# Kernel optimization log

Measured on AMD Instinct MI355X. Metric: run time of the kernel, lower is better.

The kernel has to match this reference:

```python
import jax, jax.numpy as jnp
import numpy as np

EPS = 1e-9

def squash(s, axis=-1):
    # v = (|s|^2 / (1+|s|^2)) * s/|s|
    sq_norm = jnp.sum(s * s, axis=axis, keepdims=True)
    scale = sq_norm / (1.0 + sq_norm) / jnp.sqrt(sq_norm + EPS)
    return scale * s

def setup_inputs() -> dict:
    key = jax.random.key(0)
    k1, k2 = jax.random.split(key)
    B, N, Din = 256, 1152, 8   # batch, input caps, input cap dim
    C, U = 10, 16              # output caps, output cap dim
    inputs = jax.random.normal(k1, (B, N, Din), dtype=jnp.float32)
    # 'uniform' keras initializer ~ U(-0.05, 0.05)
    W = jax.random.uniform(k2, (C, N, Din, U), dtype=jnp.float32, minval=-0.05, maxval=0.05)
    return {"inputs": inputs, "W": W}

ROUTING_ITERATIONS = 3

def reference(inputs, W):
    B = inputs.shape[0]
    C = W.shape[0]
    N = W.shape[1]
    # prediction vectors u_hat: (B, C, N, U)
    u_hat = jnp.einsum('bni,cniu->bcnu', inputs, W)
    # coupling logits b: ones, shape (B, C, N) (trailing singleton dropped)
    b = jnp.ones((B, C, N), dtype=inputs.dtype)
    out = None
    for i in range(ROUTING_ITERATIONS):
        # softmax over input-capsule axis (axis=-2 of (B,C,N,1) == N)
        c = jax.nn.softmax(b, axis=-1)  # (B, C, N)
        s = jnp.einsum('bcnu,bcn->bcu', u_hat, c)  # weighted sum over input caps
        out = squash(s, axis=-1)  # (B, C, U)
        if i < ROUTING_ITERATIONS - 1:
            # agreement: u_hat . v
            b = b + jnp.einsum('bcnu,bcu->bcn', u_hat, out)
    return out
```

## Files before the change

kernel.cpp:

```cpp
#include <hip/hip_runtime.h>
#include <math.h>


#define BATCH 256
#define CAPS  10
#define NIN   1152
#define DIN   8
#define UDIM  16
#define TPB   512
#define KITER 9

__global__ __launch_bounds__(TPB, 1) void capsule_routing_kernel(
    const float* __restrict__ x,
    const float* __restrict__ W,
    float* __restrict__ out)
{
    const int gblk = blockIdx.x;
    const int c    = gblk >> 8;
    const int b    = gblk & 255;
    const int t    = threadIdx.x;
    const int ub   = (t & 3) << 2;
    const int gg   = t >> 2;
    const int wave = t >> 6;

    __shared__ float x_s[NIN * DIN];
    __shared__ float b_s[NIN];
    __shared__ float redB[8];
    __shared__ float ps[8][UDIM];
    __shared__ float v_s[UDIM];

    {
        const float4* xg = (const float4*)(x + (size_t)b * (NIN * DIN));
        float4* xs = (float4*)x_s;
        #pragma unroll
        for (int i = 0; i < 5; ++i) {
            const int idx = t + TPB * i;
            if (idx < (NIN * DIN / 4)) xs[idx] = xg[idx];
        }
    }
    for (int n = t; n < NIN; n += TPB) b_s[n] = 1.0f;
    __syncthreads();

    const float* Wc = W + (size_t)c * (NIN * DIN * UDIM);

    float4 uh0, uh1, uh2, uh3, uh4, uh5, uh6, uh7, uh8;

#define UHCOMP(K, DST) { \
    const int n = gg + 128 * (K); \
    const float4* wr = (const float4*)(Wc + n * (DIN * UDIM) + ub); \
    const float4 xa = ((const float4*)(x_s + n * DIN))[0]; \
    const float4 xb = ((const float4*)(x_s + n * DIN))[1]; \
    float4 w0 = wr[0], w1 = wr[4], w2 = wr[8], w3 = wr[12]; \
    float4 acc; \
    acc.x = xa.x * w0.x + xa.y * w1.x + xa.z * w2.x + xa.w * w3.x; \
    acc.y = xa.x * w0.y + xa.y * w1.y + xa.z * w2.y + xa.w * w3.y; \
    acc.z = xa.x * w0.z + xa.y * w1.z + xa.z * w2.z + xa.w * w3.z; \
    acc.w = xa.x * w0.w + xa.y * w1.w + xa.z * w2.w + xa.w * w3.w; \
    w0 = wr[16]; w1 = wr[20]; w2 = wr[24]; w3 = wr[28]; \
    acc.x += xb.x * w0.x + xb.y * w1.x + xb.z * w2.x + xb.w * w3.x; \
    acc.y += xb.x * w0.y + xb.y * w1.y + xb.z * w2.y + xb.w * w3.y; \
    acc.z += xb.x * w0.z + xb.y * w1.z + xb.z * w2.z + xb.w * w3.z; \
    acc.w += xb.x * w0.w + xb.y * w1.w + xb.z * w2.w + xb.w * w3.w; \
    DST = acc; } \
    __builtin_amdgcn_sched_barrier(0);

    UHCOMP(0, uh0)
    UHCOMP(1, uh1)
    UHCOMP(2, uh2)
    UHCOMP(3, uh3)
    UHCOMP(4, uh4)
    UHCOMP(5, uh5)
    UHCOMP(6, uh6)
    UHCOMP(7, uh7)
    UHCOMP(8, uh8)

    for (int it = 0; it < 3; ++it) {
        float le = 0.f;
        float4 p; p.x = p.y = p.z = p.w = 0.f;

#define ACCP(K, UH) { \
        const float e = expf(b_s[gg + 128 * (K)]); \
        le += e; \
        p.x += e * UH.x; p.y += e * UH.y; p.z += e * UH.z; p.w += e * UH.w; }

        ACCP(0, uh0) ACCP(1, uh1) ACCP(2, uh2)
        ACCP(3, uh3) ACCP(4, uh4) ACCP(5, uh5)
        ACCP(6, uh6) ACCP(7, uh7) ACCP(8, uh8)

        #pragma unroll
        for (int mk = 1; mk <= 32; mk <<= 1) le += __shfl_xor(le, mk);
        if ((t & 63) == 0) redB[wave] = le;

        #pragma unroll
        for (int mk = 4; mk <= 32; mk <<= 1) {
            p.x += __shfl_xor(p.x, mk); p.y += __shfl_xor(p.y, mk);
            p.z += __shfl_xor(p.z, mk); p.w += __shfl_xor(p.w, mk);
        }
        if ((t & 63) < 4) {
            ps[wave][ub + 0] = p.x; ps[wave][ub + 1] = p.y;
            ps[wave][ub + 2] = p.z; ps[wave][ub + 3] = p.w;
        }
        __syncthreads();

        if (t < UDIM) {
            float esum = 0.f;
            #pragma unroll
            for (int w = 0; w < 8; ++w) esum += redB[w];
            const float inv = 4.0f / esum;
            float s = 0.f;
            #pragma unroll
            for (int w = 0; w < 8; ++w) s += ps[w][t];
            s *= inv;
            float sq = s * s;
            #pragma unroll
            for (int mk = 1; mk <= 8; mk <<= 1) sq += __shfl_xor(sq, mk);
            const float scale = sq / ((1.0f + sq) * sqrtf(sq + 1e-9f));
            const float v = scale * s;
            v_s[t] = v;
            if (it == 2) out[((size_t)b * CAPS + c) * UDIM + t] = v;
        }
        __syncthreads();

        if (it < 2) {
            const float4 v4 = *(const float4*)(v_s + ub);

#define BUPD(K, UH) { \
            float q = UH.x * v4.x + UH.y * v4.y + UH.z * v4.z + UH.w * v4.w; \
            q += __shfl_xor(q, 1); \
            q += __shfl_xor(q, 2); \
            if ((t & 3) == 0) b_s[gg + 128 * (K)] += q; }

            BUPD(0, uh0) BUPD(1, uh1) BUPD(2, uh2)
            BUPD(3, uh3) BUPD(4, uh4) BUPD(5, uh5)
            BUPD(6, uh6) BUPD(7, uh7) BUPD(8, uh8)
            __syncthreads();
        }
    }
}

extern "C" void kernel_launch(void* const* d_in, const int* in_sizes, int n_in,
                              void* d_out, int out_size, void* d_ws, size_t ws_size,
                              hipStream_t stream) {
    const float* x = (const float*)d_in[0];
    const float* W = (const float*)d_in[1];
    float* out = (float*)d_out;
    capsule_routing_kernel<<<BATCH * CAPS, TPB, 0, stream>>>(x, W, out);
}
```

Before: 130.9 us.

## Process two batch rows per block, keep routing logits in registers

Each block now handles two batch items for one output capsule, so every W load is reused for two u_hat computations and W traffic is halved. The x staging into shared memory is dropped in favour of direct global loads, and the routing logits b live in registers instead of shared memory. The first iteration is specialised to a plain sum with a constant 1/1152 scale, which is valid because the logits start uniform. Register pressure roughly doubles, and launch_bounds is raised to 4 blocks per SM, which may force spills.

Result: slower. 157.9 us (+20.6%).

```diff
diff --git a/kernel.cpp b/kernel.cpp
--- a/kernel.cpp
+++ b/kernel.cpp
@@ -8,134 +8,178 @@
 #define DIN   8
 #define UDIM  16
 #define TPB   512
-#define KITER 9
 
-__global__ __launch_bounds__(TPB, 1) void capsule_routing_kernel(
+__global__ __launch_bounds__(TPB, 4) void capsule_routing_kernel(
     const float* __restrict__ x,
     const float* __restrict__ W,
     float* __restrict__ out)
 {
     const int gblk = blockIdx.x;
-    const int c    = gblk >> 8;
-    const int b    = gblk & 255;
+    const int c    = gblk >> 7;
+    const int bp   = gblk & 127;
+    const int b0   = bp << 1;
     const int t    = threadIdx.x;
     const int ub   = (t & 3) << 2;
     const int gg   = t >> 2;
     const int wave = t >> 6;
 
-    __shared__ float x_s[NIN * DIN];
-    __shared__ float b_s[NIN];
-    __shared__ float redB[8];
-    __shared__ float ps[8][UDIM];
-    __shared__ float v_s[UDIM];
-
-    {
-        const float4* xg = (const float4*)(x + (size_t)b * (NIN * DIN));
-        float4* xs = (float4*)x_s;
-        #pragma unroll
-        for (int i = 0; i < 5; ++i) {
-            const int idx = t + TPB * i;
-            if (idx < (NIN * DIN / 4)) xs[idx] = xg[idx];
-        }
-    }
-    for (int n = t; n < NIN; n += TPB) b_s[n] = 1.0f;
-    __syncthreads();
+    __shared__ float redB[2][8];
+    __shared__ float ps[2][8][UDIM];
+    __shared__ float v_s[2][UDIM];
 
     const float* Wc = W + (size_t)c * (NIN * DIN * UDIM);
+    const float* xA = x + (size_t)b0 * (NIN * DIN);
+    const float* xB = xA + (NIN * DIN);
 
-    float4 uh0, uh1, uh2, uh3, uh4, uh5, uh6, uh7, uh8;
+    float4 uA0,uA1,uA2,uA3,uA4,uA5,uA6,uA7,uA8;
+    float4 uB0,uB1,uB2,uB3,uB4,uB5,uB6,uB7,uB8;
+    float bA0,bA1,bA2,bA3,bA4,bA5,bA6,bA7,bA8;
+    float bB0,bB1,bB2,bB3,bB4,bB5,bB6,bB7,bB8;
 
-#define UHCOMP(K, DST) { \
-    const int n = gg + 128 * (K); \
-    const float4* wr = (const float4*)(Wc + n * (DIN * UDIM) + ub); \
-    const float4 xa = ((const float4*)(x_s + n * DIN))[0]; \
-    const float4 xb = ((const float4*)(x_s + n * DIN))[1]; \
-    float4 w0 = wr[0], w1 = wr[4], w2 = wr[8], w3 = wr[12]; \
-    float4 acc; \
-    acc.x = xa.x * w0.x + xa.y * w1.x + xa.z * w2.x + xa.w * w3.x; \
-    acc.y = xa.x * w0.y + xa.y * w1.y + xa.z * w2.y + xa.w * w3.y; \
-    acc.z = xa.x * w0.z + xa.y * w1.z + xa.z * w2.z + xa.w * w3.z; \
-    acc.w = xa.x * w0.w + xa.y * w1.w + xa.z * w2.w + xa.w * w3.w; \
-    w0 = wr[16]; w1 = wr[20]; w2 = wr[24]; w3 = wr[28]; \
-    acc.x += xb.x * w0.x + xb.y * w1.x + xb.z * w2.x + xb.w * w3.x; \
-    acc.y += xb.x * w0.y + xb.y * w1.y + xb.z * w2.y + xb.w * w3.y; \
-    acc.z += xb.x * w0.z + xb.y * w1.z + xb.z * w2.z + xb.w * w3.z; \
-    acc.w += xb.x * w0.w + xb.y * w1.w + xb.z * w2.w + xb.w * w3.w; \
-    DST = acc; } \
-    __builtin_amdgcn_sched_barrier(0);
+#define UHC(K, DA, DB) { \
+    const int n_ = gg + 128 * (K); \
+    const float4* wr_ = (const float4*)(Wc + n_ * (DIN * UDIM) + ub); \
+    const float4 xa_ = ((const float4*)(xA + n_ * DIN))[0]; \
+    const float4 xb_ = ((const float4*)(xA + n_ * DIN))[1]; \
+    const float4 ya_ = ((const float4*)(xB + n_ * DIN))[0]; \
+    const float4 yb_ = ((const float4*)(xB + n_ * DIN))[1]; \
+    float4 w0_ = wr_[0], w1_ = wr_[4], w2_ = wr_[8], w3_ = wr_[12]; \
+    float4 a_, d_; \
+    a_.x = xa_.x*w0_.x + xa_.y*w1_.x + xa_.z*w2_.x + xa_.w*w3_.x; \
+    a_.y = xa_.x*w0_.y + xa_.y*w1_.y + xa_.z*w2_.y + xa_.w*w3_.y; \
+    a_.z = xa_.x*w0_.z + xa_.y*w1_.z + xa_.z*w2_.z + xa_.w*w3_.z; \
+    a_.w = xa_.x*w0_.w + xa_.y*w1_.w + xa_.z*w2_.w + xa_.w*w3_.w; \
+    d_.x = ya_.x*w0_.x + ya_.y*w1_.x + ya_.z*w2_.x + ya_.w*w3_.x; \
+    d_.y = ya_.x*w0_.y + ya_.y*w1_.y + ya_.z*w2_.y + ya_.w*w3_.y; \
+    d_.z = ya_.x*w0_.z + ya_.y*w1_.z + ya_.z*w2_.z + ya_.w*w3_.z; \
+    d_.w = ya_.x*w0_.w + ya_.y*w1_.w + ya_.z*w2_.w + ya_.w*w3_.w; \
+    w0_ = wr_[16]; w1_ = wr_[20]; w2_ = wr_[24]; w3_ = wr_[28]; \
+    a_.x += xb_.x*w0_.x + xb_.y*w1_.x + xb_.z*w2_.x + xb_.w*w3_.x; \
+    a_.y += xb_.x*w0_.y + xb_.y*w1_.y + xb_.z*w2_.y + xb_.w*w3_.y; \
+    a_.z += xb_.x*w0_.z + xb_.y*w1_.z + xb_.z*w2_.z + xb_.w*w3_.z; \
+    a_.w += xb_.x*w0_.w + xb_.y*w1_.w + xb_.z*w2_.w + xb_.w*w3_.w; \
+    d_.x += yb_.x*w0_.x + yb_.y*w1_.x + yb_.z*w2_.x + yb_.w*w3_.x; \
+    d_.y += yb_.x*w0_.y + yb_.y*w1_.y + yb_.z*w2_.y + yb_.w*w3_.y; \
+    d_.z += yb_.x*w0_.z + yb_.y*w1_.z + yb_.z*w2_.z + yb_.w*w3_.z; \
+    d_.w += yb_.x*w0_.w + yb_.y*w1_.w + yb_.z*w2_.w + yb_.w*w3_.w; \
+    DA = a_; DB = d_; }
 
-    UHCOMP(0, uh0)
-    UHCOMP(1, uh1)
-    UHCOMP(2, uh2)
-    UHCOMP(3, uh3)
-    UHCOMP(4, uh4)
-    UHCOMP(5, uh5)
-    UHCOMP(6, uh6)
-    UHCOMP(7, uh7)
-    UHCOMP(8, uh8)
+    UHC(0, uA0, uB0)
+    UHC(1, uA1, uB1)
+    UHC(2, uA2, uB2)
+    UHC(3, uA3, uB3)
+    UHC(4, uA4, uB4)
+    UHC(5, uA5, uB5)
+    UHC(6, uA6, uB6)
+    UHC(7, uA7, uB7)
+    UHC(8, uA8, uB8)
 
-    for (int it = 0; it < 3; ++it) {
-        float le = 0.f;
-        float4 p; p.x = p.y = p.z = p.w = 0.f;
+    float4 pA, pB;
+    float leA, leB;
 
-#define ACCP(K, UH) { \
-        const float e = expf(b_s[gg + 128 * (K)]); \
-        le += e; \
-        p.x += e * UH.x; p.y += e * UH.y; p.z += e * UH.z; p.w += e * UH.w; }
+#define PSTAGE(MK) { \
+    pA.x += __shfl_xor(pA.x, MK); pA.y += __shfl_xor(pA.y, MK); \
+    pA.z += __shfl_xor(pA.z, MK); pA.w += __shfl_xor(pA.w, MK); \
+    pB.x += __shfl_xor(pB.x, MK); pB.y += __shfl_xor(pB.y, MK); \
+    pB.z += __shfl_xor(pB.z, MK); pB.w += __shfl_xor(pB.w, MK); }
 
-        ACCP(0, uh0) ACCP(1, uh1) ACCP(2, uh2)
-        ACCP(3, uh3) ACCP(4, uh4) ACCP(5, uh5)
-        ACCP(6, uh6) ACCP(7, uh7) ACCP(8, uh8)
+#define PRED_WRITE() { \
+    PSTAGE(4) PSTAGE(8) PSTAGE(16) PSTAGE(32) \
+    if ((t & 63) < 4) { \
+        ps[0][wave][ub+0] = pA.x; ps[0][wave][ub+1] = pA.y; \
+        ps[0][wave][ub+2] = pA.z; ps[0][wave][ub+3] = pA.w; \
+        ps[1][wave][ub+0] = pB.x; ps[1][wave][ub+1] = pB.y; \
+        ps[1][wave][ub+2] = pB.z; ps[1][wave][ub+3] = pB.w; \
+    } }
 
-        #pragma unroll
-        for (int mk = 1; mk <= 32; mk <<= 1) le += __shfl_xor(le, mk);
-        if ((t & 63) == 0) redB[wave] = le;
+#define SQUASH(USE_RED, WROUT) { \
+    __syncthreads(); \
+    if (t < 32) { \
+        const int bi_ = t >> 4, u_ = t & 15; \
+        float inv_; \
+        if (USE_RED) { \
+            float es_ = 0.f; \
+            es_ += redB[bi_][0]; es_ += redB[bi_][1]; es_ += redB[bi_][2]; es_ += redB[bi_][3]; \
+            es_ += redB[bi_][4]; es_ += redB[bi_][5]; es_ += redB[bi_][6]; es_ += redB[bi_][7]; \
+            inv_ = 4.0f / es_;                \
+        } else { \
+            inv_ = 1.0f / 1152.0f;            \
+        } \
+        float s_ = 0.f; \
+        s_ += ps[bi_][0][u_]; s_ += ps[bi_][1][u_]; s_ += ps[bi_][2][u_]; s_ += ps[bi_][3][u_]; \
+        s_ += ps[bi_][4][u_]; s_ += ps[bi_][5][u_]; s_ += ps[bi_][6][u_]; s_ += ps[bi_][7][u_]; \
+        s_ *= inv_; \
+        float sq_ = s_ * s_; \
+        sq_ += __shfl_xor(sq_, 1); sq_ += __shfl_xor(sq_, 2); \
+        sq_ += __shfl_xor(sq_, 4); sq_ += __shfl_xor(sq_, 8); \
+        const float sc_ = sq_ / ((1.0f + sq_) * sqrtf(sq_ + 1e-9f)); \
+        const float v_ = sc_ * s_; \
+        v_s[bi_][u_] = v_; \
+        if (WROUT) out[((size_t)(b0 + bi_) * CAPS + c) * UDIM + u_] = v_; \
+    } \
+    __syncthreads(); }
 
-        #pragma unroll
-        for (int mk = 4; mk <= 32; mk <<= 1) {
-            p.x += __shfl_xor(p.x, mk); p.y += __shfl_xor(p.y, mk);
-            p.z += __shfl_xor(p.z, mk); p.w += __shfl_xor(p.w, mk);
-        }
-        if ((t & 63) < 4) {
-            ps[wave][ub + 0] = p.x; ps[wave][ub + 1] = p.y;
-            ps[wave][ub + 2] = p.z; ps[wave][ub + 3] = p.w;
-        }
-        __syncthreads();
+#define BUP(UA, UB, BA, BB, INIT) { \
+    float qa_ = UA.x*vA_.x + UA.y*vA_.y + UA.z*vA_.z + UA.w*vA_.w; \
+    float qb_ = UB.x*vB_.x + UB.y*vB_.y + UB.z*vB_.z + UB.w*vB_.w; \
+    qa_ += __shfl_xor(qa_, 1); qa_ += __shfl_xor(qa_, 2); \
+    qb_ += __shfl_xor(qb_, 1); qb_ += __shfl_xor(qb_, 2); \
+    if (INIT) { BA = 1.0f + qa_; BB = 1.0f + qb_; } \
+    else      { BA += qa_;       BB += qb_; } }
 
-        if (t < UDIM) {
-            float esum = 0.f;
-            #pragma unroll
-            for (int w = 0; w < 8; ++w) esum += redB[w];
-            const float inv = 4.0f / esum;
-            float s = 0.f;
-            #pragma unroll
-            for (int w = 0; w < 8; ++w) s += ps[w][t];
-            s *= inv;
-            float sq = s * s;
-            #pragma unroll
-            for (int mk = 1; mk <= 8; mk <<= 1) sq += __shfl_xor(sq, mk);
-            const float scale = sq / ((1.0f + sq) * sqrtf(sq + 1e-9f));
-            const float v = scale * s;
-            v_s[t] = v;
-            if (it == 2) out[((size_t)b * CAPS + c) * UDIM + t] = v;
-        }
-        __syncthreads();
+#define BUPD_ALL(INIT) { \
+    const float4 vA_ = *(const float4*)(&v_s[0][ub]); \
+    const float4 vB_ = *(const float4*)(&v_s[1][ub]); \
+    BUP(uA0, uB0, bA0, bB0, INIT) BUP(uA1, uB1, bA1, bB1, INIT) \
+    BUP(uA2, uB2, bA2, bB2, INIT) BUP(uA3, uB3, bA3, bB3, INIT) \
+    BUP(uA4, uB4, bA4, bB4, INIT) BUP(uA5, uB5, bA5, bB5, INIT) \
+    BUP(uA6, uB6, bA6, bB6, INIT) BUP(uA7, uB7, bA7, bB7, INIT) \
+    BUP(uA8, uB8, bA8, bB8, INIT) }
 
-        if (it < 2) {
-            const float4 v4 = *(const float4*)(v_s + ub);
+#define PADD(UA, UB) { \
+    pA.x += UA.x; pA.y += UA.y; pA.z += UA.z; pA.w += UA.w; \
+    pB.x += UB.x; pB.y += UB.y; pB.z += UB.z; pB.w += UB.w; }
 
-#define BUPD(K, UH) { \
-            float q = UH.x * v4.x + UH.y * v4.y + UH.z * v4.z + UH.w * v4.w; \
-            q += __shfl_xor(q, 1); \
-            q += __shfl_xor(q, 2); \
-            if ((t & 3) == 0) b_s[gg + 128 * (K)] += q; }
+#define ACCE(UA, UB, BA, BB) { \
+    const float eA_ = expf(BA); const float eB_ = expf(BB); \
+    leA += eA_; leB += eB_; \
+    pA.x += eA_*UA.x; pA.y += eA_*UA.y; pA.z += eA_*UA.z; pA.w += eA_*UA.w; \
+    pB.x += eB_*UB.x; pB.y += eB_*UB.y; pB.z += eB_*UB.z; pB.w += eB_*UB.w; }
 
-            BUPD(0, uh0) BUPD(1, uh1) BUPD(2, uh2)
-            BUPD(3, uh3) BUPD(4, uh4) BUPD(5, uh5)
-            BUPD(6, uh6) BUPD(7, uh7) BUPD(8, uh8)
-            __syncthreads();
-        }
-    }
+#define LERED_WRITE() { \
+    leA += __shfl_xor(leA, 1);  leB += __shfl_xor(leB, 1); \
+    leA += __shfl_xor(leA, 2);  leB += __shfl_xor(leB, 2); \
+    leA += __shfl_xor(leA, 4);  leB += __shfl_xor(leB, 4); \
+    leA += __shfl_xor(leA, 8);  leB += __shfl_xor(leB, 8); \
+    leA += __shfl_xor(leA, 16); leB += __shfl_xor(leB, 16); \
+    leA += __shfl_xor(leA, 32); leB += __shfl_xor(leB, 32); \
+    if ((t & 63) == 0) { redB[0][wave] = leA; redB[1][wave] = leB; } }
+
+    pA = uA0; pB = uB0;
+    PADD(uA1, uB1) PADD(uA2, uB2) PADD(uA3, uB3) PADD(uA4, uB4)
+    PADD(uA5, uB5) PADD(uA6, uB6) PADD(uA7, uB7) PADD(uA8, uB8)
+    PRED_WRITE()
+    SQUASH(0, 0)
+    BUPD_ALL(1)
+
+    leA = 0.f; leB = 0.f;
+    pA = make_float4(0.f, 0.f, 0.f, 0.f); pB = make_float4(0.f, 0.f, 0.f, 0.f);
+    ACCE(uA0, uB0, bA0, bB0) ACCE(uA1, uB1, bA1, bB1) ACCE(uA2, uB2, bA2, bB2)
+    ACCE(uA3, uB3, bA3, bB3) ACCE(uA4, uB4, bA4, bB4) ACCE(uA5, uB5, bA5, bB5)
+    ACCE(uA6, uB6, bA6, bB6) ACCE(uA7, uB7, bA7, bB7) ACCE(uA8, uB8, bA8, bB8)
+    LERED_WRITE()
+    PRED_WRITE()
+    SQUASH(1, 0)
+    BUPD_ALL(0)
+
+    leA = 0.f; leB = 0.f;
+    pA = make_float4(0.f, 0.f, 0.f, 0.f); pB = make_float4(0.f, 0.f, 0.f, 0.f);
+    ACCE(uA0, uB0, bA0, bB0) ACCE(uA1, uB1, bA1, bB1) ACCE(uA2, uB2, bA2, bB2)
+    ACCE(uA3, uB3, bA3, bB3) ACCE(uA4, uB4, bA4, bB4) ACCE(uA5, uB5, bA5, bB5)
+    ACCE(uA6, uB6, bA6, bB6) ACCE(uA7, uB7, bA7, bB7) ACCE(uA8, uB8, bA8, bB8)
+    LERED_WRITE()
+    PRED_WRITE()
+    SQUASH(1, 1)
 }
 
 extern "C" void kernel_launch(void* const* d_in, const int* in_sizes, int n_in,
@@ -144,5 +188,5 @@
     const float* x = (const float*)d_in[0];
     const float* W = (const float*)d_in[1];
     float* out = (float*)d_out;
-    capsule_routing_kernel<<<BATCH * CAPS, TPB, 0, stream>>>(x, W, out);
+    capsule_routing_kernel<<<CAPS * (BATCH / 2), TPB, 0, stream>>>(x, W, out);
 }
```
